# Kernel optimization log

Hardware: AMD Instinct MI355X
Metric: run time of the kernel (lower is better)

Reference implementation:

```python
import jax, jax.numpy as jnp
import numpy as np

N, E, H = 4096, 32768, 8
D0, C1, C2, C3 = 256, 448, 384, 256
K, M, G = 4, 500, 2000
NEG = 0.2   # GATConv LeakyReLU negative slope
EPS = 1e-5  # LayerNorm eps


def _gat(x, src, dst, W, a_s, a_d, b, heads, out_ch, concat):
    # PyG GATConv (self-loops already appended to src/dst by caller).
    n = x.shape[0]
    xp = (x @ W).reshape(n, heads, out_ch)                 # [N,H,C]
    s = jnp.einsum('nhc,hc->nh', xp, a_s)                  # alpha_src per node
    d = jnp.einsum('nhc,hc->nh', xp, a_d)                  # alpha_dst per node
    e = jax.nn.leaky_relu(s[src] + d[dst], NEG)            # [E,H]
    m = jax.ops.segment_max(e, dst, num_segments=n)
    m = jnp.where(jnp.isfinite(m), m, 0.0)
    p = jnp.exp(e - m[dst])
    z = jax.ops.segment_sum(p, dst, num_segments=n)
    alpha = p / (z[dst] + 1e-16)                           # per-dst softmax
    out = jax.ops.segment_sum(alpha[:, :, None] * xp[src], dst, num_segments=n)
    out = out.reshape(n, heads * out_ch) if concat else out[:, 0, :]
    return out + b


def _ln(x, g, b):
    mu = x.mean(-1, keepdims=True)
    v = ((x - mu) ** 2).mean(-1, keepdims=True)
    return (x - mu) * jax.lax.rsqrt(v + EPS) * g + b


def setup_inputs() -> dict:
    key = jax.random.key(0)
    ks = jax.random.split(key, 20)
    sc = 0.05
    inp = {
        'x': jax.random.normal(ks[0], (N, D0), jnp.float32),
        'edge_index': jax.random.randint(ks[1], (2, E), 0, N, jnp.int32),
        'W1': jax.random.normal(ks[2], (D0, H * C1), jnp.float32) * sc,
        'as1': jax.random.normal(ks[3], (H, C1), jnp.float32) * sc,
        'ad1': jax.random.normal(ks[4], (H, C1), jnp.float32) * sc,
        'b1': jnp.zeros((H * C1,), jnp.float32),
        'g1': jnp.ones((H * C1,), jnp.float32),
        'be1': jnp.zeros((H * C1,), jnp.float32),
        'W2': jax.random.normal(ks[5], (H * C1, H * C2), jnp.float32) * sc,
        'as2': jax.random.normal(ks[6], (H, C2), jnp.float32) * sc,
        'ad2': jax.random.normal(ks[7], (H, C2), jnp.float32) * sc,
        'b2': jnp.zeros((H * C2,), jnp.float32),
        'g2': jnp.ones((H * C2,), jnp.float32),
        'be2': jnp.zeros((H * C2,), jnp.float32),
        'W3': jax.random.normal(ks[8], (H * C2, H * C3), jnp.float32) * sc,
        'as3': jax.random.normal(ks[9], (H, C3), jnp.float32) * sc,
        'ad3': jax.random.normal(ks[10], (H, C3), jnp.float32) * sc,
        'b3': jnp.zeros((H * C3,), jnp.float32),
        'g3': jnp.ones((H * C3,), jnp.float32),
        'be3': jnp.zeros((H * C3,), jnp.float32),
        'Wh': jax.random.normal(ks[11], (K, H * C3, M), jnp.float32) * sc,
        'ash': jax.random.normal(ks[12], (K, 1, M), jnp.float32) * sc,
        'adh': jax.random.normal(ks[13], (K, 1, M), jnp.float32) * sc,
        'bh': jnp.zeros((K, M), jnp.float32),
        'idx': jnp.arange(G, dtype=jnp.int32).reshape(K, M),
    }
    return inp


def reference(x, edge_index, W1, as1, ad1, b1, g1, be1, W2, as2, ad2, b2, g2, be2,
              W3, as3, ad3, b3, g3, be3, Wh, ash, adh, bh, idx):
    n = x.shape[0]
    # eval mode: dropout_edge is identity; PyG GATConv adds self-loops
    loops = jnp.arange(n, dtype=edge_index.dtype)
    src = jnp.concatenate([edge_index[0], loops])
    dst = jnp.concatenate([edge_index[1], loops])

    h = jax.nn.relu(_gat(x, src, dst, W1, as1, ad1, b1, H, C1, True))
    h = _ln(h, g1, be1)
    h = jax.nn.relu(_gat(h, src, dst, W2, as2, ad2, b2, H, C2, True))
    h = _ln(h, g2, be2)
    h = jax.nn.relu(_gat(h, src, dst, W3, as3, ad3, b3, H, C3, True))
    h = _ln(h, g3, be3)

    per_head = jax.vmap(
        lambda Wk, ak_s, ak_d, bk: _gat(h, src, dst, Wk, ak_s, ak_d, bk, 1, M, False)
    )(Wh, ash, adh, bh)                                    # [K,N,M]

    vals = per_head.transpose(1, 0, 2).reshape(n, K * M)   # [N, G] in head order
    full = jnp.zeros((n, G), vals.dtype).at[:, idx.reshape(-1)].set(vals)
    return full, per_head
```

## Files before the change

### kernel.cpp

```cpp
#include <hip/hip_runtime.h>

#define NN 4096
#define EE 32768
#define ETOT (EE + NN)
#define HH 8
#define KK 4
#define MM 500
#define GG 2000
#define NEGS 0.2f
#define LNEPS 1e-5f

typedef unsigned short ushort;
typedef _Float16 half_t;
typedef __attribute__((ext_vector_type(8))) _Float16 half8;
typedef __attribute__((ext_vector_type(4))) _Float16 half4;
typedef __attribute__((ext_vector_type(4))) float floatx4;


__device__ __forceinline__ void get_edge(const int* __restrict__ ei, int e, int& s, int& d) {
    if (e < EE) { s = ei[e]; d = ei[EE + e]; }
    else        { s = e - EE; d = e - EE; }
}

__device__ __forceinline__ half_t f2h(float x) { return (half_t)x; }

__device__ __forceinline__ void async_lds16(const half_t* g, half_t* l) {
    __builtin_amdgcn_global_load_lds(
        (const __attribute__((address_space(1))) unsigned int*)(const void*)g,
        (__attribute__((address_space(3))) unsigned int*)(void*)l,
        16, 0, 0);
}


__global__ void k_count(const int* __restrict__ ei, int* deg) {
    int e = blockIdx.x * 256 + threadIdx.x;
    if (e < ETOT) { int s, d; get_edge(ei, e, s, d); atomicAdd(&deg[d], 1); }
}

__global__ void k_scan(const int* __restrict__ deg, int* rs, int n) {
    __shared__ int sums[1024];
    int tid = threadIdx.x;
    int base = tid * 4;
    int loc[4]; int s = 0;
    #pragma unroll
    for (int i = 0; i < 4; i++) {
        int v = (base + i < n) ? deg[base + i] : 0;
        loc[i] = s; s += v;
    }
    sums[tid] = s;
    __syncthreads();
    for (int off = 1; off < 1024; off <<= 1) {
        int v = (tid >= off) ? sums[tid - off] : 0;
        __syncthreads();
        sums[tid] += v;
        __syncthreads();
    }
    int prev = (tid > 0) ? sums[tid - 1] : 0;
    #pragma unroll
    for (int i = 0; i < 4; i++)
        if (base + i < n) rs[base + i] = prev + loc[i];
    if (tid == 1023) rs[n] = sums[1023];
}

__global__ void k_fill(const int* __restrict__ ei, const int* __restrict__ rs,
                       int* cur, int* csr_src) {
    int e = blockIdx.x * 256 + threadIdx.x;
    if (e < ETOT) {
        int s, d; get_edge(ei, e, s, d);
        int pos = rs[d] + atomicAdd(&cur[d], 1);
        csr_src[pos] = s;
    }
}


__global__ void k_f2h4(const floatx4* __restrict__ in, half4* __restrict__ out, int n4) {
    int i = blockIdx.x * 256 + threadIdx.x;
    if (i < n4) {
        floatx4 v = in[i];
        half4 o;
        o[0] = f2h(v[0]); o[1] = f2h(v[1]); o[2] = f2h(v[2]); o[3] = f2h(v[3]);
        out[i] = o;
    }
}


__global__ __launch_bounds__(256) void k_wt(const float* __restrict__ W,
                                            half_t* __restrict__ Wt,
                                            int Kd, int Nvalid, int ldw,
                                            long long sW, long long sWt) {
    __shared__ float t[32][33];
    const float* Wp = W + (size_t)blockIdx.z * sW;
    half_t* Wtp = Wt + (size_t)blockIdx.z * sWt;
    int n0 = blockIdx.x * 32, k0 = blockIdx.y * 32;
    int tx = threadIdx.x & 31, ty = threadIdx.x >> 5;
    #pragma unroll
    for (int i = 0; i < 32; i += 8)
        t[ty + i][tx] = (n0 + tx < Nvalid) ? Wp[(size_t)(k0 + ty + i) * ldw + n0 + tx] : 0.f;
    __syncthreads();
    #pragma unroll
    for (int i = 0; i < 32; i += 8)
        Wtp[(size_t)(n0 + ty + i) * Kd + k0 + tx] = f2h(t[tx][ty + i]);
}


#define BM 128
#define BN 128
#define BK 64

__global__ __launch_bounds__(256) void k_gemm_mfma(
    const half_t* __restrict__ A,
    const half_t* __restrict__ Bt,
    half_t* __restrict__ C,
    int Kd, int Nreal, int ldc,
    long long strideBt, long long strideC)
{
    __shared__ __align__(16) half_t As[BM * BK];
    __shared__ __align__(16) half_t Bs[BN * BK];

    const half_t* Btp = Bt + (size_t)blockIdx.z * strideBt;
    half_t* Cp = C + (size_t)blockIdx.z * strideC;
    int col0 = blockIdx.x * BN, row0 = blockIdx.y * BM;

    int lane = threadIdx.x & 63;
    int wave = threadIdx.x >> 6;
    int wm = (wave >> 1) * 64, wn = (wave & 1) * 64;

    int srow = wave * 32 + (lane >> 3);
    int gchunk = (lane & 7) ^ ((lane >> 3) & 7);
    const half_t* ga = A   + (size_t)(row0 + srow) * Kd + gchunk * 8;
    const half_t* gb = Btp + (size_t)(col0 + srow) * Kd + gchunk * 8;
    half_t* lA = &As[(wave * 32) * BK];
    half_t* lB = &Bs[(wave * 32) * BK];

    int r = lane & 15;
    int rx = r & 7;

    floatx4 acc[4][4];
    #pragma unroll
    for (int i = 0; i < 4; i++)
        #pragma unroll
        for (int j = 0; j < 4; j++) acc[i][j] = (floatx4){0.f, 0.f, 0.f, 0.f};

    for (int k0 = 0; k0 < Kd; k0 += BK) {
        #pragma unroll
        for (int j = 0; j < 4; j++) {
            async_lds16(ga + k0 + (size_t)(j * 8) * Kd, lA + (j * 8) * BK);
            async_lds16(gb + k0 + (size_t)(j * 8) * Kd, lB + (j * 8) * BK);
        }
        __syncthreads();
        #pragma unroll
        for (int kk = 0; kk < BK; kk += 32) {
            int phys = (((kk >> 3) + (lane >> 4)) ^ rx) << 3;
            half8 a[4], b[4];
            #pragma unroll
            for (int i = 0; i < 4; i++)
                a[i] = *(const half8*)&As[(wm + i * 16 + r) * BK + phys];
            #pragma unroll
            for (int j = 0; j < 4; j++)
                b[j] = *(const half8*)&Bs[(wn + j * 16 + r) * BK + phys];
            #pragma unroll
            for (int i = 0; i < 4; i++)
                #pragma unroll
                for (int j = 0; j < 4; j++)
                    acc[i][j] = __builtin_amdgcn_mfma_f32_16x16x32_f16(a[i], b[j], acc[i][j], 0, 0, 0);
        }
        __syncthreads();
    }

    int q4 = (lane >> 4) * 4;
    #pragma unroll
    for (int i = 0; i < 4; i++) {
        #pragma unroll
        for (int rr = 0; rr < 4; rr++) {
            int row = row0 + wm + i * 16 + q4 + rr;
            #pragma unroll
            for (int j = 0; j < 4; j++) {
                int col = col0 + wn + j * 16 + (lane & 15);
                if (col < Nreal) Cp[(size_t)row * ldc + col] = f2h(acc[i][j][rr]);
            }
        }
    }
}


__global__ void k_sd(const half_t* __restrict__ xp, const float* __restrict__ as_,
                     const float* __restrict__ ad_, float* s, float* d, int H, int C) {
    int n = blockIdx.x / H, h = blockIdx.x % H;
    int lane = threadIdx.x;
    const half4* row4 = (const half4*)(xp + (size_t)n * H * C + (size_t)h * C);
    const float* av = as_ + (size_t)h * C;
    const float* bv = ad_ + (size_t)h * C;
    int C4 = C >> 2;
    float ss = 0.f, dd = 0.f;
    for (int c4 = lane; c4 < C4; c4 += 64) {
        half4 v = row4[c4];
        floatx4 a = *(const floatx4*)(av + c4 * 4);
        floatx4 b = *(const floatx4*)(bv + c4 * 4);
        float x0 = (float)v[0], x1 = (float)v[1], x2 = (float)v[2], x3 = (float)v[3];
        ss += x0 * a[0] + x1 * a[1] + x2 * a[2] + x3 * a[3];
        dd += x0 * b[0] + x1 * b[1] + x2 * b[2] + x3 * b[3];
    }
    #pragma unroll
    for (int o = 32; o > 0; o >>= 1) {
        ss += __shfl_down(ss, o, 64);
        dd += __shfl_down(dd, o, 64);
    }
    if (lane == 0) { s[n * H + h] = ss; d[n * H + h] = dd; }
}


__global__ __launch_bounds__(256) void k_agg_ln(
    const half_t* __restrict__ xp, const float* __restrict__ s, const float* __restrict__ d,
    const int* __restrict__ csr_src, const int* __restrict__ rs,
    const float* __restrict__ bias, const float* __restrict__ gam,
    const float* __restrict__ bet, half_t* __restrict__ outh, int H, int C) {
    __shared__ int sh_src[256];
    __shared__ float sh_w[256 * HH];
    __shared__ float sh_d[HH];
    __shared__ float sh_z[HH];
    __shared__ float red[256];
    __shared__ float red2[256];
    int n = blockIdx.x, tid = threadIdx.x;
    int Dout = H * C;
    int NCH = Dout >> 3;
    int CCH = C >> 3;
    int start = rs[n], end = rs[n + 1];
    if (tid < H) { sh_d[tid] = d[(size_t)n * H + tid]; sh_z[tid] = 0.f; }
    float acc[2][8];
    #pragma unroll
    for (int a = 0; a < 2; a++)
        #pragma unroll
        for (int e = 0; e < 8; e++) acc[a][e] = 0.f;

    for (int e0 = start; e0 < end; e0 += 256) {
        int cnt = min(256, end - e0);
        if (tid < cnt) sh_src[tid] = csr_src[e0 + tid];
        __syncthreads();
        for (int i = tid; i < cnt * H; i += 256) {
            int ei = i / H, h = i - ei * H;
            float v = s[(size_t)sh_src[ei] * H + h] + sh_d[h];
            v = (v >= 0.f) ? v : NEGS * v;
            sh_w[i] = expf(v);
        }
        __syncthreads();
        if (tid < H) {
            float zz = 0.f;
            for (int i = 0; i < cnt; i++) zz += sh_w[i * H + tid];
            sh_z[tid] += zz;
        }
        int ai = 0;
        for (int ch = tid; ch < NCH; ch += 256, ai++) {
            int h = ch / CCH;
            float a0 = acc[ai][0], a1 = acc[ai][1], a2 = acc[ai][2], a3 = acc[ai][3];
            float a4 = acc[ai][4], a5 = acc[ai][5], a6 = acc[ai][6], a7 = acc[ai][7];
            for (int i = 0; i < cnt; i++) {
                float w = sh_w[i * H + h];
                half8 v = *(const half8*)(xp + (size_t)sh_src[i] * Dout + (ch << 3));
                a0 += w * (float)v[0]; a1 += w * (float)v[1];
                a2 += w * (float)v[2]; a3 += w * (float)v[3];
                a4 += w * (float)v[4]; a5 += w * (float)v[5];
                a6 += w * (float)v[6]; a7 += w * (float)v[7];
            }
            acc[ai][0] = a0; acc[ai][1] = a1; acc[ai][2] = a2; acc[ai][3] = a3;
            acc[ai][4] = a4; acc[ai][5] = a5; acc[ai][6] = a6; acc[ai][7] = a7;
        }
        __syncthreads();
    }

    float vals[2][8];
    float sum = 0.f, sumsq = 0.f;
    int ai = 0;
    for (int ch = tid; ch < NCH; ch += 256, ai++) {
        int h = ch / CCH;
        float zi = 1.f / (sh_z[h] + 1e-16f);
        #pragma unroll
        for (int e = 0; e < 8; e++) {
            float v = acc[ai][e] * zi + bias[(ch << 3) + e];
            v = fmaxf(v, 0.f);
            vals[ai][e] = v;
            sum += v; sumsq += v * v;
        }
    }
    red[tid] = sum; red2[tid] = sumsq;
    __syncthreads();
    for (int o = 128; o > 0; o >>= 1) {
        if (tid < o) { red[tid] += red[tid + o]; red2[tid] += red2[tid + o]; }
        __syncthreads();
    }
    float mu = red[0] / Dout;
    float var = red2[0] / Dout - mu * mu;
    float rstd = rsqrtf(var + LNEPS);
    ai = 0;
    for (int ch = tid; ch < NCH; ch += 256, ai++) {
        half8 o;
        #pragma unroll
        for (int e = 0; e < 8; e++)
            o[e] = f2h((vals[ai][e] - mu) * rstd * gam[(ch << 3) + e] + bet[(ch << 3) + e]);
        *(half8*)(outh + (size_t)n * Dout + (ch << 3)) = o;
    }
}


__global__ __launch_bounds__(256) void k_agg_head(
    const half_t* __restrict__ xp, const float* __restrict__ s, const float* __restrict__ d,
    const int* __restrict__ csr_src, const int* __restrict__ rs,
    const float* __restrict__ bias, const int* __restrict__ idxm,
    float* out_full, float* out_ph) {
    __shared__ int sh_src[256];
    __shared__ float sh_w[256 * KK];
    __shared__ float sh_d[KK];
    __shared__ float sh_z[KK];
    int n = blockIdx.x, tid = threadIdx.x;
    const int Dout = KK * MM;
    const int NCH = Dout >> 3;
    int start = rs[n], end = rs[n + 1];
    if (tid < KK) { sh_d[tid] = d[(size_t)n * KK + tid]; sh_z[tid] = 0.f; }
    float acc[8];
    #pragma unroll
    for (int e = 0; e < 8; e++) acc[e] = 0.f;
    int ch = tid;
    int cb = ch << 3;

    for (int e0 = start; e0 < end; e0 += 256) {
        int cnt = min(256, end - e0);
        if (tid < cnt) sh_src[tid] = csr_src[e0 + tid];
        __syncthreads();
        for (int i = tid; i < cnt * KK; i += 256) {
            int ei = i / KK, k = i - ei * KK;
            float v = s[(size_t)sh_src[ei] * KK + k] + sh_d[k];
            v = (v >= 0.f) ? v : NEGS * v;
            sh_w[i] = expf(v);
        }
        __syncthreads();
        if (tid < KK) {
            float zz = 0.f;
            for (int i = 0; i < cnt; i++) zz += sh_w[i * KK + tid];
            sh_z[tid] += zz;
        }
        if (ch < NCH) {
            for (int i = 0; i < cnt; i++) {
                const float* wv = &sh_w[i * KK];
                half8 v = *(const half8*)(xp + (size_t)sh_src[i] * Dout + cb);
                #pragma unroll
                for (int e = 0; e < 8; e++)
                    acc[e] += wv[(cb + e) / MM] * (float)v[e];
            }
        }
        __syncthreads();
    }
    if (ch < NCH) {
        #pragma unroll
        for (int e = 0; e < 8; e++) {
            int c = cb + e;
            int k = c / MM, m = c - k * MM;
            float v = acc[e] / (sh_z[k] + 1e-16f) + bias[c];
            out_ph[((size_t)k * NN + n) * MM + m] = v;
            out_full[(size_t)n * GG + idxm[c]] = v;
        }
    }
}


extern "C" void kernel_launch(void* const* d_in, const int* in_sizes, int n_in,
                              void* d_out, int out_size, void* d_ws, size_t ws_size,
                              hipStream_t stream) {
    (void)in_sizes; (void)n_in; (void)out_size; (void)ws_size;
    const float* x   = (const float*)d_in[0];
    const int*   ei  = (const int*)d_in[1];
    const float* W1  = (const float*)d_in[2];
    const float* as1 = (const float*)d_in[3];
    const float* ad1 = (const float*)d_in[4];
    const float* b1  = (const float*)d_in[5];
    const float* g1  = (const float*)d_in[6];
    const float* be1 = (const float*)d_in[7];
    const float* W2  = (const float*)d_in[8];
    const float* as2 = (const float*)d_in[9];
    const float* ad2 = (const float*)d_in[10];
    const float* b2  = (const float*)d_in[11];
    const float* g2  = (const float*)d_in[12];
    const float* be2 = (const float*)d_in[13];
    const float* W3  = (const float*)d_in[14];
    const float* as3 = (const float*)d_in[15];
    const float* ad3 = (const float*)d_in[16];
    const float* b3  = (const float*)d_in[17];
    const float* g3  = (const float*)d_in[18];
    const float* be3 = (const float*)d_in[19];
    const float* Wh  = (const float*)d_in[20];
    const float* ash = (const float*)d_in[21];
    const float* adh = (const float*)d_in[22];
    const float* bh  = (const float*)d_in[23];
    const int*   idxm = (const int*)d_in[24];
    float* out = (float*)d_out;

    char* w = (char*)d_ws;
    auto carve = [&](size_t bytes) { char* p = w; w += (bytes + 255) & ~(size_t)255; return p; };
    half_t* xp16    = (half_t*)carve((size_t)NN * 3584 * 2);
    half_t* Wt      = (half_t*)carve((size_t)3072 * 3584 * 2);
    float*  sarr    = (float*)carve((size_t)NN * HH * 4);
    float*  darr    = (float*)carve((size_t)NN * HH * 4);
    int*    csr_src = (int*)carve((size_t)ETOT * 4);
    int*    rowst   = (int*)carve((size_t)(NN + 1) * 4);
    int*    cur     = (int*)carve((size_t)NN * 4);
    half_t* Ah = (half_t*)d_out;

    hipMemsetAsync(cur, 0, (size_t)NN * 4, stream);
    k_count<<<(ETOT + 255) / 256, 256, 0, stream>>>(ei, cur);
    k_scan<<<1, 1024, 0, stream>>>(cur, rowst, NN);
    hipMemsetAsync(cur, 0, (size_t)NN * 4, stream);
    k_fill<<<(ETOT + 255) / 256, 256, 0, stream>>>(ei, rowst, cur, csr_src);

    k_f2h4<<<(NN * 64 + 255) / 256, 256, 0, stream>>>(
        (const floatx4*)x, (half4*)Ah, NN * 64);

    auto gat = [&](const float* W, const float* as_, const float* ad_,
                   const float* bias, const float* gam, const float* bet, int Din, int C) {
        int Dout = HH * C;
        k_wt<<<dim3(Dout / 32, Din / 32, 1), 256, 0, stream>>>(W, Wt, Din, Dout, Dout, 0, 0);
        k_gemm_mfma<<<dim3(Dout / BN, NN / BM, 1), 256, 0, stream>>>(
            Ah, Wt, xp16, Din, Dout, Dout, 0, 0);
        k_sd<<<NN * HH, 64, 0, stream>>>(xp16, as_, ad_, sarr, darr, HH, C);
        k_agg_ln<<<NN, 256, 0, stream>>>(xp16, sarr, darr, csr_src, rowst,
                                         bias, gam, bet, Ah, HH, C);
    };
    gat(W1, as1, ad1, b1, g1, be1, 256,  448);
    gat(W2, as2, ad2, b2, g2, be2, 3584, 384);
    gat(W3, as3, ad3, b3, g3, be3, 3072, 256);

    k_wt<<<dim3(512 / 32, 2048 / 32, KK), 256, 0, stream>>>(
        Wh, Wt, 2048, MM, MM, (long long)2048 * MM, (long long)512 * 2048);
    k_gemm_mfma<<<dim3(512 / BN, NN / BM, KK), 256, 0, stream>>>(
        Ah, Wt, xp16, 2048, MM, GG, (long long)512 * 2048, (long long)MM);
    k_sd<<<NN * KK, 64, 0, stream>>>(xp16, ash, adh, sarr, darr, KK, MM);
    k_agg_head<<<NN, 256, 0, stream>>>(xp16, sarr, darr, csr_src, rowst,
                                       bh, idxm, out, out + (size_t)NN * GG);
}
```

Before: 639.9 us.

## Fuse setup kernels and overlap next-layer weight transpose with score kernel

The scan kernel now zeroes the degree counter itself, which removes a memset, and the CSR fill is merged with the fp32-to-fp16 conversion of x. The per-node attention-score kernel is packed four wavefronts per block. It is also launched as one grid together with the next layer's weight transpose, so the transpose runs alongside the score computation instead of as its own launch. This cuts launch count and small-kernel tail latency. The risk is that the transpose now writes into the shared Wt buffer after the current GEMM has consumed it, so correctness depends on stream ordering.

Result: no change. 644.5 us (+0.7%).

```diff
diff --git a/kernel.cpp b/kernel.cpp
--- a/kernel.cpp
+++ b/kernel.cpp
@@ -37,7 +37,7 @@
     if (e < ETOT) { int s, d; get_edge(ei, e, s, d); atomicAdd(&deg[d], 1); }
 }
 
-__global__ void k_scan(const int* __restrict__ deg, int* rs, int n) {
+__global__ void k_scan(int* deg, int* rs, int n) {
     __shared__ int sums[1024];
     int tid = threadIdx.x;
     int base = tid * 4;
@@ -47,6 +47,9 @@
         int v = (base + i < n) ? deg[base + i] : 0;
         loc[i] = s; s += v;
     }
+    #pragma unroll
+    for (int i = 0; i < 4; i++)
+        if (base + i < n) deg[base + i] = 0;
     sums[tid] = s;
     __syncthreads();
     for (int off = 1; off < 1024; off <<= 1) {
@@ -62,25 +65,90 @@
     if (tid == 1023) rs[n] = sums[1023];
 }
 
-__global__ void k_fill(const int* __restrict__ ei, const int* __restrict__ rs,
-                       int* cur, int* csr_src) {
-    int e = blockIdx.x * 256 + threadIdx.x;
-    if (e < ETOT) {
-        int s, d; get_edge(ei, e, s, d);
+__global__ void k_fill_f2h(const int* __restrict__ ei, const int* __restrict__ rs,
+                           int* cur, int* csr_src,
+                           const floatx4* __restrict__ x4, half4* __restrict__ xh4) {
+    int i = blockIdx.x * 256 + threadIdx.x;
+    if (i < ETOT) {
+        int s, d; get_edge(ei, i, s, d);
         int pos = rs[d] + atomicAdd(&cur[d], 1);
         csr_src[pos] = s;
     }
-}
-
-
-__global__ void k_f2h4(const floatx4* __restrict__ in, half4* __restrict__ out, int n4) {
-    int i = blockIdx.x * 256 + threadIdx.x;
-    if (i < n4) {
-        floatx4 v = in[i];
+    if (i < NN * 64) {
+        floatx4 v = x4[i];
         half4 o;
         o[0] = f2h(v[0]); o[1] = f2h(v[1]); o[2] = f2h(v[2]); o[3] = f2h(v[3]);
-        out[i] = o;
-    }
+        xh4[i] = o;
+    }
+}
+
+
+__device__ __forceinline__ void sd_body(const half_t* __restrict__ xp,
+                                        const float* __restrict__ as_,
+                                        const float* __restrict__ ad_,
+                                        float* s, float* d, int H, int C,
+                                        int idx, int lane) {
+    const half4* row4 = (const half4*)(xp + (size_t)idx * C);
+    int h = idx % H;
+    const float* av = as_ + (size_t)h * C;
+    const float* bv = ad_ + (size_t)h * C;
+    int C4 = C >> 2;
+    float ss = 0.f, dd = 0.f;
+    for (int c4 = lane; c4 < C4; c4 += 64) {
+        half4 v = row4[c4];
+        floatx4 a = *(const floatx4*)(av + c4 * 4);
+        floatx4 b = *(const floatx4*)(bv + c4 * 4);
+        float x0 = (float)v[0], x1 = (float)v[1], x2 = (float)v[2], x3 = (float)v[3];
+        ss += x0 * a[0] + x1 * a[1] + x2 * a[2] + x3 * a[3];
+        dd += x0 * b[0] + x1 * b[1] + x2 * b[2] + x3 * b[3];
+    }
+    #pragma unroll
+    for (int o = 32; o > 0; o >>= 1) {
+        ss += __shfl_down(ss, o, 64);
+        dd += __shfl_down(dd, o, 64);
+    }
+    if (lane == 0) { s[idx] = ss; d[idx] = dd; }
+}
+
+__global__ __launch_bounds__(256) void k_sd4(const half_t* __restrict__ xp,
+                                             const float* __restrict__ as_,
+                                             const float* __restrict__ ad_,
+                                             float* s, float* d, int H, int C, int npairs) {
+    int idx = blockIdx.x * 4 + (threadIdx.x >> 6);
+    if (idx < npairs)
+        sd_body(xp, as_, ad_, s, d, H, C, idx, threadIdx.x & 63);
+}
+
+
+__global__ __launch_bounds__(256) void k_sd_wt(
+    const half_t* __restrict__ xp, const float* __restrict__ as_,
+    const float* __restrict__ ad_, float* s, float* d, int H, int C, int nsd, int npairs,
+    const float* __restrict__ W, half_t* __restrict__ Wt,
+    int Kd, int Nvalid, int ldw, long long sW, long long sWt, int wgx, int wgy) {
+    __shared__ float t[32][33];
+    int bid = blockIdx.x;
+    if (bid < nsd) {
+        int idx = bid * 4 + (threadIdx.x >> 6);
+        if (idx < npairs)
+            sd_body(xp, as_, ad_, s, d, H, C, idx, threadIdx.x & 63);
+        return;
+    }
+    int wb = bid - nsd;
+    int bx = wb % wgx;
+    int rem = wb / wgx;
+    int by = rem % wgy;
+    int bz = rem / wgy;
+    const float* Wp = W + (size_t)bz * sW;
+    half_t* Wtp = Wt + (size_t)bz * sWt;
+    int n0 = bx * 32, k0 = by * 32;
+    int tx = threadIdx.x & 31, ty = threadIdx.x >> 5;
+    #pragma unroll
+    for (int i = 0; i < 32; i += 8)
+        t[ty + i][tx] = (n0 + tx < Nvalid) ? Wp[(size_t)(k0 + ty + i) * ldw + n0 + tx] : 0.f;
+    __syncthreads();
+    #pragma unroll
+    for (int i = 0; i < 32; i += 8)
+        Wtp[(size_t)(n0 + ty + i) * Kd + k0 + tx] = f2h(t[tx][ty + i]);
 }
 
 
@@ -180,32 +248,6 @@
             }
         }
     }
-}
-
-
-__global__ void k_sd(const half_t* __restrict__ xp, const float* __restrict__ as_,
-                     const float* __restrict__ ad_, float* s, float* d, int H, int C) {
-    int n = blockIdx.x / H, h = blockIdx.x % H;
-    int lane = threadIdx.x;
-    const half4* row4 = (const half4*)(xp + (size_t)n * H * C + (size_t)h * C);
-    const float* av = as_ + (size_t)h * C;
-    const float* bv = ad_ + (size_t)h * C;
-    int C4 = C >> 2;
-    float ss = 0.f, dd = 0.f;
-    for (int c4 = lane; c4 < C4; c4 += 64) {
-        half4 v = row4[c4];
-        floatx4 a = *(const floatx4*)(av + c4 * 4);
-        floatx4 b = *(const floatx4*)(bv + c4 * 4);
-        float x0 = (float)v[0], x1 = (float)v[1], x2 = (float)v[2], x3 = (float)v[3];
-        ss += x0 * a[0] + x1 * a[1] + x2 * a[2] + x3 * a[3];
-        dd += x0 * b[0] + x1 * b[1] + x2 * b[2] + x3 * b[3];
-    }
-    #pragma unroll
-    for (int o = 32; o > 0; o >>= 1) {
-        ss += __shfl_down(ss, o, 64);
-        dd += __shfl_down(dd, o, 64);
-    }
-    if (lane == 0) { s[n * H + h] = ss; d[n * H + h] = dd; }
 }
 
 
@@ -406,31 +448,37 @@
     hipMemsetAsync(cur, 0, (size_t)NN * 4, stream);
     k_count<<<(ETOT + 255) / 256, 256, 0, stream>>>(ei, cur);
     k_scan<<<1, 1024, 0, stream>>>(cur, rowst, NN);
-    hipMemsetAsync(cur, 0, (size_t)NN * 4, stream);
-    k_fill<<<(ETOT + 255) / 256, 256, 0, stream>>>(ei, rowst, cur, csr_src);
-
-    k_f2h4<<<(NN * 64 + 255) / 256, 256, 0, stream>>>(
-        (const floatx4*)x, (half4*)Ah, NN * 64);
-
-    auto gat = [&](const float* W, const float* as_, const float* ad_,
-                   const float* bias, const float* gam, const float* bet, int Din, int C) {
-        int Dout = HH * C;
-        k_wt<<<dim3(Dout / 32, Din / 32, 1), 256, 0, stream>>>(W, Wt, Din, Dout, Dout, 0, 0);
-        k_gemm_mfma<<<dim3(Dout / BN, NN / BM, 1), 256, 0, stream>>>(
-            Ah, Wt, xp16, Din, Dout, Dout, 0, 0);
-        k_sd<<<NN * HH, 64, 0, stream>>>(xp16, as_, ad_, sarr, darr, HH, C);
-        k_agg_ln<<<NN, 256, 0, stream>>>(xp16, sarr, darr, csr_src, rowst,
-                                         bias, gam, bet, Ah, HH, C);
-    };
-    gat(W1, as1, ad1, b1, g1, be1, 256,  448);
-    gat(W2, as2, ad2, b2, g2, be2, 3584, 384);
-    gat(W3, as3, ad3, b3, g3, be3, 3072, 256);
-
-    k_wt<<<dim3(512 / 32, 2048 / 32, KK), 256, 0, stream>>>(
-        Wh, Wt, 2048, MM, MM, (long long)2048 * MM, (long long)512 * 2048);
+    k_fill_f2h<<<(NN * 64 + 255) / 256, 256, 0, stream>>>(
+        ei, rowst, cur, csr_src, (const floatx4*)x, (half4*)Ah);
+
+    k_wt<<<dim3(3584 / 32, 256 / 32, 1), 256, 0, stream>>>(W1, Wt, 256, 3584, 3584, 0, 0);
+    k_gemm_mfma<<<dim3(3584 / BN, NN / BM, 1), 256, 0, stream>>>(
+        Ah, Wt, xp16, 256, 3584, 3584, 0, 0);
+    k_sd_wt<<<8192 + 10752, 256, 0, stream>>>(
+        xp16, as1, ad1, sarr, darr, HH, 448, 8192, NN * HH,
+        W2, Wt, 3584, 3072, 3072, 0, 0, 96, 112);
+    k_agg_ln<<<NN, 256, 0, stream>>>(xp16, sarr, darr, csr_src, rowst,
+                                     b1, g1, be1, Ah, HH, 448);
+
+    k_gemm_mfma<<<dim3(3072 / BN, NN / BM, 1), 256, 0, stream>>>(
+        Ah, Wt, xp16, 3584, 3072, 3072, 0, 0);
+    k_sd_wt<<<8192 + 6144, 256, 0, stream>>>(
+        xp16, as2, ad2, sarr, darr, HH, 384, 8192, NN * HH,
+        W3, Wt, 3072, 2048, 2048, 0, 0, 64, 96);
+    k_agg_ln<<<NN, 256, 0, stream>>>(xp16, sarr, darr, csr_src, rowst,
+                                     b2, g2, be2, Ah, HH, 384);
+
+    k_gemm_mfma<<<dim3(2048 / BN, NN / BM, 1), 256, 0, stream>>>(
+        Ah, Wt, xp16, 3072, 2048, 2048, 0, 0);
+    k_sd_wt<<<8192 + 4096, 256, 0, stream>>>(
+        xp16, as3, ad3, sarr, darr, HH, 256, 8192, NN * HH,
+        Wh, Wt, 2048, MM, MM, (long long)2048 * MM, (long long)512 * 2048, 16, 64);
+    k_agg_ln<<<NN, 256, 0, stream>>>(xp16, sarr, darr, csr_src, rowst,
+                                     b3, g3, be3, Ah, HH, 256);
+
     k_gemm_mfma<<<dim3(512 / BN, NN / BM, KK), 256, 0, stream>>>(
         Ah, Wt, xp16, 2048, MM, GG, (long long)512 * 2048, (long long)MM);
-    k_sd<<<NN * KK, 64, 0, stream>>>(xp16, ash, adh, sarr, darr, KK, MM);
+    k_sd4<<<(NN * KK) / 4, 256, 0, stream>>>(xp16, ash, adh, sarr, darr, KK, MM, NN * KK);
     k_agg_head<<<NN, 256, 0, stream>>>(xp16, sarr, darr, csr_src, rowst,
                                        bh, idxm, out, out + (size_t)NN * GG);
 }
```
